# Kernel optimization log

Hardware: AMD Instinct MI355X
Metric: run time of the kernel (lower is better)

## Reference

```python
import jax, jax.numpy as jnp
import numpy as np

NUM_HEADS = 32
NUM_KV_HEADS = 8
HEAD_DIM = 96
ROPE_BASE = 10000.0


def setup_inputs() -> dict:
    key = jax.random.key(0)
    k1, k2, k3 = jax.random.split(key, 3)
    B, S, H = 2, 2048, 3072
    op_size = NUM_HEADS * HEAD_DIM + 2 * NUM_KV_HEADS * HEAD_DIM  # 4608
    hidden_states = jax.random.normal(k1, (B, S, H), dtype=jnp.float32)
    w_qkv = jax.random.normal(k2, (op_size, H), dtype=jnp.float32) * (H ** -0.5)
    w_o = jax.random.normal(k3, (H, H), dtype=jnp.float32) * (H ** -0.5)
    position_ids = jnp.broadcast_to(jnp.arange(S, dtype=jnp.int64), (B, S))
    return {"hidden_states": hidden_states, "position_ids": position_ids,
            "w_qkv": w_qkv, "w_o": w_o}


def _rotate_half(x):
    x1, x2 = jnp.split(x, 2, axis=-1)
    return jnp.concatenate((-x2, x1), axis=-1)


def reference(hidden_states, position_ids, w_qkv, w_o):
    B, S, H = hidden_states.shape
    nh, nkv, hd = NUM_HEADS, NUM_KV_HEADS, HEAD_DIM
    n_rep = nh // nkv

    # fused QKV projection (torch Linear: x @ W^T)
    qkv = jnp.einsum('bsh,oh->bso', hidden_states, w_qkv)
    q_pos = nh * hd
    q = qkv[..., :q_pos].reshape(B, S, nh, hd).transpose(0, 2, 1, 3)
    k = qkv[..., q_pos:q_pos + nkv * hd].reshape(B, S, nkv, hd).transpose(0, 2, 1, 3)
    v = qkv[..., q_pos + nkv * hd:].reshape(B, S, nkv, hd).transpose(0, 2, 1, 3)

    # rotary embedding (Phi3RotaryEmbedding, rope_scaling=None)
    inv_freq = 1.0 / (ROPE_BASE ** (jnp.arange(0, hd, 2, dtype=jnp.float32) / hd))
    freqs = position_ids.astype(jnp.float32)[:, :, None] * inv_freq[None, None, :]  # [B,S,hd/2]
    emb = jnp.concatenate((freqs, freqs), axis=-1)  # [B,S,hd]
    cos = jnp.cos(emb)[:, None, :, :]  # unsqueeze head dim
    sin = jnp.sin(emb)[:, None, :, :]
    q = q * cos + _rotate_half(q) * sin
    k = k * cos + _rotate_half(k) * sin

    # repeat_kv: (B, nkv, S, hd) -> (B, nh, S, hd)
    k = jnp.repeat(k, n_rep, axis=1)
    v = jnp.repeat(v, n_rep, axis=1)

    # causal SDPA
    scale = 1.0 / jnp.sqrt(jnp.float32(hd))
    scores = jnp.einsum('bhqd,bhkd->bhqk', q, k) * scale
    causal = jnp.tril(jnp.ones((S, S), dtype=bool))
    scores = jnp.where(causal[None, None], scores, jnp.finfo(scores.dtype).min)
    probs = jax.nn.softmax(scores, axis=-1)
    attn = jnp.einsum('bhqk,bhkd->bhqd', probs, v)  # [B,nh,S,hd]

    attn = attn.transpose(0, 2, 1, 3).reshape(B, S, nh * hd)
    return jnp.einsum('bsh,oh->bso', attn, w_o)
```

## Files before the change

kernel.cpp:

```cpp
#include <hip/hip_runtime.h>
#include <stdint.h>
#include <math.h>

#define B_   2
#define S_   2048
#define H_   3072
#define NH   32
#define NKV  8
#define HD   96
#define OPSZ 4608
#define MM   (B_*S_)

typedef __attribute__((ext_vector_type(8))) short short8;
typedef __attribute__((ext_vector_type(4))) float floatx4;

__device__ __forceinline__ short f2bf(float f) {
    union { float f; uint32_t u; } v; v.f = f;
    uint32_t r = v.u + 0x7fffu + ((v.u >> 16) & 1u);
    return (short)(r >> 16);
}
__device__ __forceinline__ float bf2f(short s) {
    union { uint32_t u; float f; } v; v.u = ((uint32_t)(uint16_t)s) << 16;
    return v.f;
}
__device__ __forceinline__ uint32_t pk_bf_trunc(float lo, float hi) {
    union { float f; uint32_t u; } a, b; a.f = lo; b.f = hi;
    return (a.u >> 16) | (b.u & 0xFFFF0000u);
}
__device__ __forceinline__ float fast_exp2(float x) {
    float r;
    asm volatile("v_exp_f32 %0, %1" : "=v"(r) : "v"(x));
    return r;
}
__device__ __forceinline__ float dpp_max16(float x) {
    union { float f; int i; } a, t;
    a.f = x;
    t.i = __builtin_amdgcn_update_dpp(0, a.i, 0x128, 0xF, 0xF, false); a.f = fmaxf(a.f, t.f);
    t.i = __builtin_amdgcn_update_dpp(0, a.i, 0x124, 0xF, 0xF, false); a.f = fmaxf(a.f, t.f);
    t.i = __builtin_amdgcn_update_dpp(0, a.i, 0x122, 0xF, 0xF, false); a.f = fmaxf(a.f, t.f);
    t.i = __builtin_amdgcn_update_dpp(0, a.i, 0x121, 0xF, 0xF, false); a.f = fmaxf(a.f, t.f);
    return a.f;
}

__device__ __forceinline__ void async_load16(const void* g, void* l) {
    __builtin_amdgcn_global_load_lds(
        (const __attribute__((address_space(1))) void*)g,
        (__attribute__((address_space(3))) void*)l, 16, 0, 0);
}

#define CN1 (MM * H_ / 4)
#define CN2 (OPSZ * H_ / 4)
#define CN3 (H_ * H_ / 4)
__global__ void cast3_f32_bf16(const float* __restrict__ s1, const float* __restrict__ s2,
                               const float* __restrict__ s3, short* __restrict__ d1,
                               short* __restrict__ d2, short* __restrict__ d3) {
    int gid = blockIdx.x * blockDim.x + threadIdx.x;
    int stride = gridDim.x * blockDim.x;
    for (int i = gid; i < CN1; i += stride) {
        float4 v = ((const float4*)s1)[i];
        short4 o; o.x = f2bf(v.x); o.y = f2bf(v.y); o.z = f2bf(v.z); o.w = f2bf(v.w);
        ((short4*)d1)[i] = o;
    }
    for (int i = gid; i < CN2; i += stride) {
        float4 v = ((const float4*)s2)[i];
        short4 o; o.x = f2bf(v.x); o.y = f2bf(v.y); o.z = f2bf(v.z); o.w = f2bf(v.w);
        ((short4*)d2)[i] = o;
    }
    for (int i = gid; i < CN3; i += stride) {
        float4 v = ((const float4*)s3)[i];
        short4 o; o.x = f2bf(v.x); o.y = f2bf(v.y); o.z = f2bf(v.z); o.w = f2bf(v.w);
        ((short4*)d3)[i] = o;
    }
}

template<int OUT_BF16>
__global__ __launch_bounds__(512, 2) void gemm256(const short* __restrict__ A, const short* __restrict__ Bm,
                                                  float* __restrict__ Cf, short* __restrict__ Cb,
                                                  int M, int N, int K) {
    __shared__ __align__(16) char smem[131072];
    const int tid = threadIdx.x;
    const int w = tid >> 6, l = tid & 63;
    const int L15 = l & 15, quad = l >> 4;

    const int gm = M >> 8;
    const int nwg = gridDim.x;
    const int id = blockIdx.x;
    const int qq = nwg >> 3, rr = nwg & 7;
    const int xcd = id & 7, sidx = id >> 3;
    const int wgid = (xcd < rr ? xcd * (qq + 1) : rr * (qq + 1) + (xcd - rr) * qq) + sidx;
    const int m0 = (wgid % gm) << 8;
    const int n0 = (wgid / gm) << 8;
    const int wm = (w >> 2) << 7;
    const int wn = (w & 3) << 6;

    const int cbl = ((l & 3) * 16) ^ (((l >> 5) & 1) << 5);
    uint32_t aofs[4], bofs[4];
    #pragma unroll
    for (int j = 0; j < 4; j++) {
        const int s = j * 8 + w;
        const int row = ((s >> 1) << 4) + (l >> 2);
        const int colb = ((s & 1) << 6) + cbl;
        aofs[j] = (uint32_t)(m0 + row) * (uint32_t)(K * 2) + colb;
        bofs[j] = (uint32_t)(n0 + row) * (uint32_t)(K * 2) + colb;
    }
    char* ldsA = (char*)smem;
    char* ldsB = (char*)smem + 65536;
    const int dstw = w * 1024;

    const int lane_off = L15 * 64 + ((quad * 16) ^ (((L15 >> 3) & 1) << 5));
    const int aoff = (w >> 2) * 16384 + lane_off;
    const int boff = (w & 3) * 8192 + lane_off;

    floatx4 acc[8][4];
    #pragma unroll
    for (int i = 0; i < 8; i++)
        #pragma unroll
        for (int j = 0; j < 4; j++)
            acc[i][j] = (floatx4){0.f, 0.f, 0.f, 0.f};

    auto stageA = [&](int kt, int buf) {
        const uint32_t kb = (uint32_t)kt << 7;
        #pragma unroll
        for (int j = 0; j < 4; j++)
            async_load16((const char*)A + (size_t)(aofs[j] + kb), ldsA + buf * 32768 + j * 8192 + dstw);
    };
    auto stageB = [&](int kt, int buf) {
        const uint32_t kb = (uint32_t)kt << 7;
        #pragma unroll
        for (int j = 0; j < 4; j++)
            async_load16((const char*)Bm + (size_t)(bofs[j] + kb), ldsB + buf * 32768 + j * 8192 + dstw);
    };

    const int nkt = K >> 6;
    stageB(0, 0); stageA(0, 0);
    stageB(1, 1); stageA(1, 1);

    for (int t = 0; t < nkt; t++) {
        const int c = t & 1;
        const char* ab = ldsA + c * 32768 + aoff;
        const char* bb = ldsB + c * 32768 + boff;
        int nx = t + 2; if (nx >= nkt) nx -= nkt;

        asm volatile("s_waitcnt vmcnt(8)" ::: "memory");
        __builtin_amdgcn_s_barrier();
        __builtin_amdgcn_sched_barrier(0);

        short8 a0[4][2], a1[4][2], bfrag[4][2];
        #pragma unroll
        for (int i = 0; i < 4; i++)
            #pragma unroll
            for (int kk = 0; kk < 2; kk++)
                a0[i][kk] = *(const short8*)(ab + i * 2048 + kk * 1024);
        #pragma unroll
        for (int j = 0; j < 4; j++)
            #pragma unroll
            for (int kk = 0; kk < 2; kk++)
                bfrag[j][kk] = *(const short8*)(bb + j * 2048 + kk * 1024);
        __builtin_amdgcn_s_barrier();
        __builtin_amdgcn_s_setprio(1);
        #pragma unroll
        for (int kk = 0; kk < 2; kk++)
            #pragma unroll
            for (int i = 0; i < 4; i++)
                #pragma unroll
                for (int j = 0; j < 2; j++)
                    acc[i][j] = __builtin_amdgcn_mfma_f32_16x16x32_bf16(a0[i][kk], bfrag[j][kk], acc[i][j], 0, 0, 0);
        __builtin_amdgcn_s_setprio(0);
        __builtin_amdgcn_s_barrier();
        __builtin_amdgcn_s_setprio(1);
        #pragma unroll
        for (int kk = 0; kk < 2; kk++)
            #pragma unroll
            for (int i = 0; i < 4; i++)
                #pragma unroll
                for (int j = 2; j < 4; j++)
                    acc[i][j] = __builtin_amdgcn_mfma_f32_16x16x32_bf16(a0[i][kk], bfrag[j][kk], acc[i][j], 0, 0, 0);
        __builtin_amdgcn_s_setprio(0);
        #pragma unroll
        for (int i = 0; i < 4; i++)
            #pragma unroll
            for (int kk = 0; kk < 2; kk++)
                a1[i][kk] = *(const short8*)(ab + 8192 + i * 2048 + kk * 1024);
        __builtin_amdgcn_s_barrier();
        stageB(nx, c);
        __builtin_amdgcn_s_setprio(1);
        #pragma unroll
        for (int kk = 0; kk < 2; kk++)
            #pragma unroll
            for (int i = 0; i < 4; i++)
                #pragma unroll
                for (int j = 0; j < 2; j++)
                    acc[4 + i][j] = __builtin_amdgcn_mfma_f32_16x16x32_bf16(a1[i][kk], bfrag[j][kk], acc[4 + i][j], 0, 0, 0);
        __builtin_amdgcn_s_setprio(0);
        __builtin_amdgcn_s_barrier();
        stageA(nx, c);
        __builtin_amdgcn_s_setprio(1);
        #pragma unroll
        for (int kk = 0; kk < 2; kk++)
            #pragma unroll
            for (int i = 0; i < 4; i++)
                #pragma unroll
                for (int j = 2; j < 4; j++)
                    acc[4 + i][j] = __builtin_amdgcn_mfma_f32_16x16x32_bf16(a1[i][kk], bfrag[j][kk], acc[4 + i][j], 0, 0, 0);
        __builtin_amdgcn_s_setprio(0);
    }
    asm volatile("s_waitcnt vmcnt(0)" ::: "memory");

    #pragma unroll
    for (int i = 0; i < 8; i++)
        #pragma unroll
        for (int j = 0; j < 4; j++)
            #pragma unroll
            for (int r = 0; r < 4; r++) {
                const int row = m0 + wm + i * 16 + quad * 4 + r;
                const int col = n0 + wn + j * 16 + L15;
                const float v = acc[i][j][r];
                if (OUT_BF16) Cb[(size_t)row * N + col] = f2bf(v);
                else          Cf[(size_t)row * N + col] = v;
            }
}

__global__ void rope_reorder(const short* __restrict__ qkv, const int* __restrict__ pos_ids,
                             short* __restrict__ Q, short* __restrict__ Kc) {
    const int total = B_ * S_ * (NH + NKV) * HD;
    int idx = blockIdx.x * blockDim.x + threadIdx.x;
    int stride = gridDim.x * blockDim.x;
    for (; idx < total; idx += stride) {
        int d = idx % HD;
        int row = idx / HD;
        int h_all = row % (NH + NKV);
        int sb = row / (NH + NKV);
        int s = sb % S_;
        int b = sb / S_;
        int base = (b * S_ + s) * OPSZ;
        int off = (h_all < NH) ? (h_all * HD + d) : (H_ + (h_all - NH) * HD + d);
        float x = bf2f(qkv[base + off]);
        int delta = (d < 48) ? 48 : -48;
        float x2 = bf2f(qkv[base + off + delta]);
        int fi = d % 48;
        float inv = exp2f((float)fi * -0.2768273412f);
        float theta = (float)pos_ids[b * S_ + s] * inv;
        float sn, cs;
        __sincosf(theta, &sn, &cs);
        float rot = (d < 48) ? -x2 : x2;
        float outv = x * cs + rot * sn;
        if (h_all < NH) {
            outv *= 0.14724438747f;
            Q[((size_t)(b * NH + h_all) * S_ + s) * HD + d] = f2bf(outv);
        } else {
            int kvh = h_all - NH;
            size_t kaddr = ((size_t)(b * NKV + kvh) * S_ + s) * 128
                         + (((d >> 3) + s) & 15) * 8 + (d & 7);
            Kc[kaddr] = f2bf(outv);
        }
    }
}

__global__ __launch_bounds__(256) void v_transpose(const short* __restrict__ qkv, short* __restrict__ Vt) {
    __shared__ short tile[64 * 104];
    int blk = blockIdx.x;
    int st  = blk & 31;
    int kvh = (blk >> 5) & 7;
    int b   = blk >> 8;
    int s0  = st * 64;
    int tid = threadIdx.x;
    #pragma unroll
    for (int i = 0; i < 3; i++) {
        int c = tid + i * 256;
        int row = c / 12, col8 = c % 12;
        *(short8*)&tile[row * 104 + col8 * 8] =
            *(const short8*)(qkv + (size_t)(b * S_ + s0 + row) * OPSZ + 3840 + kvh * HD + col8 * 8);
    }
    __syncthreads();
    #pragma unroll
    for (int i = 0; i < 3; i++) {
        int c = tid + i * 256;
        int d = c >> 3, col8 = c & 7;
        int chunk0 = (col8 - d) & 7;
        short8 v;
        #pragma unroll
        for (int j = 0; j < 8; j++) {
            int col0 = chunk0 * 8 + j;
            int n = ((col0 >> 5) << 1) | (col0 & 1);
            int t = (col0 & 31) >> 1;
            v[j] = tile[(n * 16 + t) * 104 + d];
        }
        *(short8*)(Vt + ((size_t)(b * NKV + kvh) * HD + d) * S_ + s0 + col8 * 8) = v;
    }
}

__global__ __launch_bounds__(256) void flash_attn(const short* __restrict__ Q, const short* __restrict__ Kc,
                                                  const short* __restrict__ Vt, short* __restrict__ attn) {
    __shared__ short kl[2][64 * 128];
    __shared__ short vl[2][112 * 64];
    __shared__ short pl[4][32 * 72];
    const int x = blockIdx.x, h = blockIdx.y, b = blockIdx.z;
    const int kvh = h >> 2;
    const int tid = threadIdx.x, wave = tid >> 6, lane = tid & 63;
    const int L15 = lane & 15, quad = lane >> 4;

    #pragma unroll
    for (int i = 0; i < 2; i++) {
        uint32_t* p = (uint32_t*)&vl[i][96 * 64];
        #pragma unroll
        for (int k = 0; k < 2; k++) {
            int idx = tid + k * 256;
            p[idx] = (idx < 32) ? 0x3F803F80u : 0u;
        }
    }

    const short* kbase = Kc + (size_t)(b * NKV + kvh) * S_ * 128;
    const short* vbase = Vt + (size_t)(b * NKV + kvh) * HD * S_;
    const int klane   = lane * 8;
    const int vrow_lo = lane >> 3;
    const int vcol    = (lane & 7) * 8;

    int rotK[3], rotV[2];
    #pragma unroll
    for (int kk = 0; kk < 3; kk++) rotK[kk] = ((kk * 4 + quad + L15) & 15) * 8;
    #pragma unroll
    for (int kk = 0; kk < 2; kk++) rotV[kk] = ((kk * 4 + quad + L15) & 7) * 8;

    auto stage = [&](int kv0, int buf) {
        const short* ksrc = kbase + (size_t)kv0 * 128;
        #pragma unroll
        for (int i = 0; i < 4; i++) {
            int ck = wave * 4 + i;
            async_load16(ksrc + ck * 512 + klane, &kl[buf][ck * 512]);
        }
        #pragma unroll
        for (int i = 0; i < 3; i++) {
            int ck = wave * 3 + i;
            async_load16(vbase + (size_t)(ck * 8 + vrow_lo) * S_ + kv0 + vcol, &vl[buf][ck * 512]);
        }
    };

    #pragma unroll
    for (int pp = 0; pp < 2; pp++) {
        const int qt = pp ? x : (15 - x);
        const int q0 = qt * 128;
        const int jmax = 2 * qt + 2;

        short8 qf[2][3];
        #pragma unroll
        for (int mm = 0; mm < 2; mm++) {
            const short* qrow = Q + ((size_t)(b * NH + h) * S_ + q0 + wave * 32 + mm * 16 + L15) * HD;
            #pragma unroll
            for (int kk = 0; kk < 3; kk++) qf[mm][kk] = *(const short8*)(qrow + kk * 32 + quad * 8);
        }
        floatx4 o[2][7];
        float m_r[2][4];
        #pragma unroll
        for (int mm = 0; mm < 2; mm++) {
            #pragma unroll
            for (int nn = 0; nn < 7; nn++) o[mm][nn] = (floatx4){0.f, 0.f, 0.f, 0.f};
            #pragma unroll
            for (int r = 0; r < 4; r++) m_r[mm][r] = -3.0e38f;
        }

        __syncthreads();
        stage(0, 0);

        for (int j = 0; j < jmax; j++) {
            const int c = j & 1;
            const int kv0 = j * 64;
            __syncthreads();
            if (j + 1 < jmax) stage(kv0 + 64, 1 - c);

            const short* klp = kl[c];
            const short* vlp = vl[c];

            floatx4 sacc[2][4];
            #pragma unroll
            for (int mm = 0; mm < 2; mm++)
                #pragma unroll
                for (int n = 0; n < 4; n++) sacc[mm][n] = (floatx4){0.f, 0.f, 0.f, 0.f};
            #pragma unroll
            for (int n = 0; n < 4; n++)
                #pragma unroll
                for (int kk = 0; kk < 3; kk++) {
                    short8 kf = *(const short8*)&klp[(n * 16 + L15) * 128 + rotK[kk]];
                    sacc[0][n] = __builtin_amdgcn_mfma_f32_16x16x32_bf16(qf[0][kk], kf, sacc[0][n], 0, 0, 0);
                    sacc[1][n] = __builtin_amdgcn_mfma_f32_16x16x32_bf16(qf[1][kk], kf, sacc[1][n], 0, 0, 0);
                }

            #pragma unroll
            for (int mm = 0; mm < 2; mm++) {
                const int tbase = q0 + wave * 32 + mm * 16;
                if (kv0 + 63 > tbase) {
                    int qr_base = tbase + quad * 4;
                    #pragma unroll
                    for (int n = 0; n < 4; n++) {
                        int kv = kv0 + n * 16 + L15;
                        #pragma unroll
                        for (int r = 0; r < 4; r++)
                            if (kv > qr_base + r) sacc[mm][n][r] = -3.0e38f;
                    }
                }
                float alpha[4];
                #pragma unroll
                for (int r = 0; r < 4; r++) {
                    float mx = fmaxf(fmaxf(sacc[mm][0][r], sacc[mm][1][r]),
                                     fmaxf(sacc[mm][2][r], sacc[mm][3][r]));
                    mx = dpp_max16(mx);
                    float mn = fmaxf(m_r[mm][r], mx);
                    alpha[r] = fast_exp2(m_r[mm][r] - mn);
                    m_r[mm][r] = mn;
                }
                #pragma unroll
                for (int n = 0; n < 4; n++)
                    #pragma unroll
                    for (int r = 0; r < 4; r++)
                        sacc[mm][n][r] = fast_exp2(sacc[mm][n][r] - m_r[mm][r]);
                #pragma unroll
                for (int r = 0; r < 4; r++) {
                    int prow = mm * 16 + quad * 4 + r;
                    *(uint32_t*)&pl[wave][prow * 72 + 2 * L15]      = pk_bf_trunc(sacc[mm][0][r], sacc[mm][1][r]);
                    *(uint32_t*)&pl[wave][prow * 72 + 32 + 2 * L15] = pk_bf_trunc(sacc[mm][2][r], sacc[mm][3][r]);
                }
                #pragma unroll
                for (int nn = 0; nn < 7; nn++)
                    #pragma unroll
                    for (int r = 0; r < 4; r++) o[mm][nn][r] *= alpha[r];
            }

            #pragma unroll
            for (int kk = 0; kk < 2; kk++) {
                short8 af0 = *(const short8*)&pl[wave][L15 * 72 + kk * 32 + quad * 8];
                short8 af1 = *(const short8*)&pl[wave][(16 + L15) * 72 + kk * 32 + quad * 8];
                #pragma unroll
                for (int nn = 0; nn < 7; nn++) {
                    short8 vf = *(const short8*)&vlp[(nn * 16 + L15) * 64 + rotV[kk]];
                    o[0][nn] = __builtin_amdgcn_mfma_f32_16x16x32_bf16(af0, vf, o[0][nn], 0, 0, 0);
                    o[1][nn] = __builtin_amdgcn_mfma_f32_16x16x32_bf16(af1, vf, o[1][nn], 0, 0, 0);
                }
            }
        }

        #pragma unroll
        for (int mm = 0; mm < 2; mm++) {
            float inv_l[4];
            #pragma unroll
            for (int r = 0; r < 4; r++) {
                float l = __shfl(o[mm][6][r], lane & 48);
                inv_l[r] = 1.0f / l;
            }
            #pragma unroll
            for (int nn = 0; nn < 6; nn++)
                #pragma unroll
                for (int r = 0; r < 4; r++) {
                    float v = o[mm][nn][r] * inv_l[r];
                    int row = q0 + wave * 32 + mm * 16 + quad * 4 + r;
                    attn[((size_t)(b * S_) + row) * H_ + h * HD + nn * 16 + L15] = f2bf(v);
                }
        }
    }
}

extern "C" void kernel_launch(void* const* d_in, const int* in_sizes, int n_in,
                              void* d_out, int out_size, void* d_ws, size_t ws_size,
                              hipStream_t stream) {
    const float* hid  = (const float*)d_in[0];
    const int*   pos  = (const int*)d_in[1];
    const float* wqkv = (const float*)d_in[2];
    const float* wo   = (const float*)d_in[3];
    float* out = (float*)d_out;
    char* ws = (char*)d_ws;

    short* hid_b  = (short*)(ws + 0L);
    short* wqkv_b = (short*)(ws + 25165824L);
    short* wo_b   = (short*)(ws + 53477376L);
    short* qkv_b  = (short*)(ws + 72351744L);
    short* q_b    = (short*)(ws + 110100480L);
    short* k_b    = (short*)(ws + 135266304L);
    short* vt_b   = (short*)(ws + 143654912L);
    short* attn_b = (short*)(ws + 0L);

    cast3_f32_bf16<<<4096, 256, 0, stream>>>(hid, wqkv, wo, hid_b, wqkv_b, wo_b);

    gemm256<1><<<(OPSZ / 256) * (MM / 256), 512, 0, stream>>>(hid_b, wqkv_b, nullptr, qkv_b, MM, OPSZ, H_);

    rope_reorder<<<8192, 256, 0, stream>>>(qkv_b, pos, q_b, k_b);
    v_transpose<<<512, 256, 0, stream>>>(qkv_b, vt_b);

    flash_attn<<<dim3(8, NH, B_), 256, 0, stream>>>(q_b, k_b, vt_b, attn_b);

    gemm256<0><<<(H_ / 256) * (MM / 256), 512, 0, stream>>>(attn_b, wo_b, out, nullptr, MM, H_, H_);
}
```

Before: 552.1 us.

## Retile GEMMs to 256xBN so each grid fills exactly 256 workgroups

Replaces the fixed 256x256 GEMM tile with a templated 256xBN tile (BN=288 for the QKV projection, BN=192 for the output projection). Each GEMM now launches exactly 256 workgroups, which removes the partial wave of the old 288- and 192-block grids on a 256-CU part. The warp layout changes to 4x2 with a 4xNF accumulator grid, and the main loop is rescheduled into three B-fragment groups with fewer barriers. Prefetching stops wrapping around at the end of K. The trade-offs are uneven per-warp B loads when BSUB is not a multiple of 8, and different LDS and register pressure.

```diff
diff --git a/kernel.cpp b/kernel.cpp
--- a/kernel.cpp
+++ b/kernel.cpp
@@ -73,14 +73,21 @@
     }
 }
 
-template<int OUT_BF16>
-__global__ __launch_bounds__(512, 2) void gemm256(const short* __restrict__ A, const short* __restrict__ Bm,
-                                                  float* __restrict__ Cf, short* __restrict__ Cb,
-                                                  int M, int N, int K) {
-    __shared__ __align__(16) char smem[131072];
+template<int BN, int OUT_BF16>
+__global__ __launch_bounds__(512, 2) void gemmN(const short* __restrict__ A, const short* __restrict__ Bm,
+                                                float* __restrict__ Cf, short* __restrict__ Cb,
+                                                int M, int N, int K) {
+    constexpr int NF    = BN / 32;
+    constexpr int G     = NF / 3;
+    constexpr int BSUB  = BN / 8;
+    constexpr int BBY   = BN * 128;
+    constexpr int JB    = (BSUB + 7) / 8;
+    constexpr int VMN   = (BN == 288) ? 8 : 7;
+    __shared__ __align__(16) char smem[65536 + 2 * BBY];
     const int tid = threadIdx.x;
     const int w = tid >> 6, l = tid & 63;
     const int L15 = l & 15, quad = l >> 4;
+    const int wr = w & 3, wc = w >> 2;
 
     const int gm = M >> 8;
     const int nwg = gridDim.x;
@@ -89,46 +96,53 @@
     const int xcd = id & 7, sidx = id >> 3;
     const int wgid = (xcd < rr ? xcd * (qq + 1) : rr * (qq + 1) + (xcd - rr) * qq) + sidx;
     const int m0 = (wgid % gm) << 8;
-    const int n0 = (wgid / gm) << 8;
-    const int wm = (w >> 2) << 7;
-    const int wn = (w & 3) << 6;
+    const int n0 = (wgid / gm) * BN;
 
     const int cbl = ((l & 3) * 16) ^ (((l >> 5) & 1) << 5);
-    uint32_t aofs[4], bofs[4];
+    uint32_t aofs[4], bofs[JB];
     #pragma unroll
     for (int j = 0; j < 4; j++) {
         const int s = j * 8 + w;
         const int row = ((s >> 1) << 4) + (l >> 2);
         const int colb = ((s & 1) << 6) + cbl;
         aofs[j] = (uint32_t)(m0 + row) * (uint32_t)(K * 2) + colb;
+    }
+    #pragma unroll
+    for (int j = 0; j < JB; j++) {
+        const int s = j * 8 + w;
+        const int sc = (s < BSUB) ? s : 0;
+        const int row = ((sc >> 1) << 4) + (l >> 2);
+        const int colb = ((sc & 1) << 6) + cbl;
         bofs[j] = (uint32_t)(n0 + row) * (uint32_t)(K * 2) + colb;
     }
     char* ldsA = (char*)smem;
     char* ldsB = (char*)smem + 65536;
-    const int dstw = w * 1024;
 
     const int lane_off = L15 * 64 + ((quad * 16) ^ (((L15 >> 3) & 1) << 5));
-    const int aoff = (w >> 2) * 16384 + lane_off;
-    const int boff = (w & 3) * 8192 + lane_off;
-
-    floatx4 acc[8][4];
-    #pragma unroll
-    for (int i = 0; i < 8; i++)
-        #pragma unroll
-        for (int j = 0; j < 4; j++)
+    const int aoff = (wr * 4) * 2048 + lane_off;
+    const int boff = (wc * NF) * 2048 + lane_off;
+
+    floatx4 acc[4][NF];
+    #pragma unroll
+    for (int i = 0; i < 4; i++)
+        #pragma unroll
+        for (int j = 0; j < NF; j++)
             acc[i][j] = (floatx4){0.f, 0.f, 0.f, 0.f};
 
     auto stageA = [&](int kt, int buf) {
         const uint32_t kb = (uint32_t)kt << 7;
         #pragma unroll
         for (int j = 0; j < 4; j++)
-            async_load16((const char*)A + (size_t)(aofs[j] + kb), ldsA + buf * 32768 + j * 8192 + dstw);
+            async_load16((const char*)A + (size_t)(aofs[j] + kb),
+                         ldsA + buf * 32768 + (j * 8 + w) * 1024);
     };
     auto stageB = [&](int kt, int buf) {
         const uint32_t kb = (uint32_t)kt << 7;
         #pragma unroll
-        for (int j = 0; j < 4; j++)
-            async_load16((const char*)Bm + (size_t)(bofs[j] + kb), ldsB + buf * 32768 + j * 8192 + dstw);
+        for (int j = 0; j < JB; j++)
+            if (j * 8 + w < BSUB)
+                async_load16((const char*)Bm + (size_t)(bofs[j] + kb),
+                             ldsB + buf * BBY + (j * 8 + w) * 1024);
     };
 
     const int nkt = K >> 6;
@@ -138,82 +152,76 @@
     for (int t = 0; t < nkt; t++) {
         const int c = t & 1;
         const char* ab = ldsA + c * 32768 + aoff;
-        const char* bb = ldsB + c * 32768 + boff;
-        int nx = t + 2; if (nx >= nkt) nx -= nkt;
-
-        asm volatile("s_waitcnt vmcnt(8)" ::: "memory");
+        const char* bb = ldsB + c * BBY + boff;
+
+        if (BN == 288) asm volatile("s_waitcnt vmcnt(8)" ::: "memory");
+        else           asm volatile("s_waitcnt vmcnt(7)" ::: "memory");
         __builtin_amdgcn_s_barrier();
         __builtin_amdgcn_sched_barrier(0);
 
-        short8 a0[4][2], a1[4][2], bfrag[4][2];
+        short8 a[4][2], bg0[G][2], bg1[G][2], bg2[G][2];
         #pragma unroll
         for (int i = 0; i < 4; i++)
             #pragma unroll
             for (int kk = 0; kk < 2; kk++)
-                a0[i][kk] = *(const short8*)(ab + i * 2048 + kk * 1024);
-        #pragma unroll
-        for (int j = 0; j < 4; j++)
+                a[i][kk] = *(const short8*)(ab + i * 2048 + kk * 1024);
+        #pragma unroll
+        for (int g = 0; g < G; g++)
             #pragma unroll
             for (int kk = 0; kk < 2; kk++)
-                bfrag[j][kk] = *(const short8*)(bb + j * 2048 + kk * 1024);
+                bg0[g][kk] = *(const short8*)(bb + g * 2048 + kk * 1024);
+        #pragma unroll
+        for (int g = 0; g < G; g++)
+            #pragma unroll
+            for (int kk = 0; kk < 2; kk++)
+                bg1[g][kk] = *(const short8*)(bb + (G + g) * 2048 + kk * 1024);
+        __builtin_amdgcn_s_setprio(1);
+        #pragma unroll
+        for (int kk = 0; kk < 2; kk++)
+            #pragma unroll
+            for (int i = 0; i < 4; i++)
+                #pragma unroll
+                for (int g = 0; g < G; g++)
+                    acc[i][g] = __builtin_amdgcn_mfma_f32_16x16x32_bf16(a[i][kk], bg0[g][kk], acc[i][g], 0, 0, 0);
+        __builtin_amdgcn_s_setprio(0);
+        #pragma unroll
+        for (int g = 0; g < G; g++)
+            #pragma unroll
+            for (int kk = 0; kk < 2; kk++)
+                bg2[g][kk] = *(const short8*)(bb + (2 * G + g) * 2048 + kk * 1024);
+        __builtin_amdgcn_s_setprio(1);
+        #pragma unroll
+        for (int kk = 0; kk < 2; kk++)
+            #pragma unroll
+            for (int i = 0; i < 4; i++)
+                #pragma unroll
+                for (int g = 0; g < G; g++)
+                    acc[i][G + g] = __builtin_amdgcn_mfma_f32_16x16x32_bf16(a[i][kk], bg1[g][kk], acc[i][G + g], 0, 0, 0);
+        __builtin_amdgcn_s_setprio(0);
+        __builtin_amdgcn_sched_barrier(0);
         __builtin_amdgcn_s_barrier();
+        __builtin_amdgcn_sched_barrier(0);
+        if (t + 2 < nkt) { stageB(t + 2, c); stageA(t + 2, c); }
         __builtin_amdgcn_s_setprio(1);
         #pragma unroll
         for (int kk = 0; kk < 2; kk++)
             #pragma unroll
             for (int i = 0; i < 4; i++)
                 #pragma unroll
-                for (int j = 0; j < 2; j++)
-                    acc[i][j] = __builtin_amdgcn_mfma_f32_16x16x32_bf16(a0[i][kk], bfrag[j][kk], acc[i][j], 0, 0, 0);
+                for (int g = 0; g < G; g++)
+                    acc[i][2 * G + g] = __builtin_amdgcn_mfma_f32_16x16x32_bf16(a[i][kk], bg2[g][kk], acc[i][2 * G + g], 0, 0, 0);
         __builtin_amdgcn_s_setprio(0);
-        __builtin_amdgcn_s_barrier();
-        __builtin_amdgcn_s_setprio(1);
-        #pragma unroll
-        for (int kk = 0; kk < 2; kk++)
-            #pragma unroll
-            for (int i = 0; i < 4; i++)
-                #pragma unroll
-                for (int j = 2; j < 4; j++)
-                    acc[i][j] = __builtin_amdgcn_mfma_f32_16x16x32_bf16(a0[i][kk], bfrag[j][kk], acc[i][j], 0, 0, 0);
-        __builtin_amdgcn_s_setprio(0);
-        #pragma unroll
-        for (int i = 0; i < 4; i++)
-            #pragma unroll
-            for (int kk = 0; kk < 2; kk++)
-                a1[i][kk] = *(const short8*)(ab + 8192 + i * 2048 + kk * 1024);
-        __builtin_amdgcn_s_barrier();
-        stageB(nx, c);
-        __builtin_amdgcn_s_setprio(1);
-        #pragma unroll
-        for (int kk = 0; kk < 2; kk++)
-            #pragma unroll
-            for (int i = 0; i < 4; i++)
-                #pragma unroll
-                for (int j = 0; j < 2; j++)
-                    acc[4 + i][j] = __builtin_amdgcn_mfma_f32_16x16x32_bf16(a1[i][kk], bfrag[j][kk], acc[4 + i][j], 0, 0, 0);
-        __builtin_amdgcn_s_setprio(0);
-        __builtin_amdgcn_s_barrier();
-        stageA(nx, c);
-        __builtin_amdgcn_s_setprio(1);
-        #pragma unroll
-        for (int kk = 0; kk < 2; kk++)
-            #pragma unroll
-            for (int i = 0; i < 4; i++)
-                #pragma unroll
-                for (int j = 2; j < 4; j++)
-                    acc[4 + i][j] = __builtin_amdgcn_mfma_f32_16x16x32_bf16(a1[i][kk], bfrag[j][kk], acc[4 + i][j], 0, 0, 0);
-        __builtin_amdgcn_s_setprio(0);
     }
     asm volatile("s_waitcnt vmcnt(0)" ::: "memory");
 
     #pragma unroll
-    for (int i = 0; i < 8; i++)
-        #pragma unroll
-        for (int j = 0; j < 4; j++)
+    for (int i = 0; i < 4; i++)
+        #pragma unroll
+        for (int j = 0; j < NF; j++)
             #pragma unroll
             for (int r = 0; r < 4; r++) {
-                const int row = m0 + wm + i * 16 + quad * 4 + r;
-                const int col = n0 + wn + j * 16 + L15;
+                const int row = m0 + wr * 64 + i * 16 + quad * 4 + r;
+                const int col = n0 + wc * (BN / 2) + j * 16 + L15;
                 const float v = acc[i][j][r];
                 if (OUT_BF16) Cb[(size_t)row * N + col] = f2bf(v);
                 else          Cf[(size_t)row * N + col] = v;
@@ -478,12 +486,12 @@
 
     cast3_f32_bf16<<<4096, 256, 0, stream>>>(hid, wqkv, wo, hid_b, wqkv_b, wo_b);
 
-    gemm256<1><<<(OPSZ / 256) * (MM / 256), 512, 0, stream>>>(hid_b, wqkv_b, nullptr, qkv_b, MM, OPSZ, H_);
+    gemmN<288, 1><<<256, 512, 0, stream>>>(hid_b, wqkv_b, nullptr, qkv_b, MM, OPSZ, H_);
 
     rope_reorder<<<8192, 256, 0, stream>>>(qkv_b, pos, q_b, k_b);
     v_transpose<<<512, 256, 0, stream>>>(qkv_b, vt_b);
 
     flash_attn<<<dim3(8, NH, B_), 256, 0, stream>>>(q_b, k_b, vt_b, attn_b);
 
-    gemm256<0><<<(H_ / 256) * (MM / 256), 512, 0, stream>>>(attn_b, wo_b, out, nullptr, MM, H_, H_);
-}
+    gemmN<192, 0><<<256, 512, 0, stream>>>(attn_b, wo_b, out, nullptr, MM, H_, H_);
+}
```

Result: faster. 474.8 us (-14.0%).
